# Kernel tuning notes

Measured on AMD Instinct MI355X. Metric: run time of the kernel, lower is better.

The kernel has to match this reference:

```python
import jax, jax.numpy as jnp
import numpy as np

EPS = 1e-6
GROUPS = 32


def group_norm(x, scale, bias):
    # x: [b, c, d, h, w]
    b, c, d, h, w = x.shape
    xg = x.reshape(b, GROUPS, c // GROUPS, d, h, w)
    mean = xg.mean(axis=(2, 3, 4, 5), keepdims=True)
    var = xg.var(axis=(2, 3, 4, 5), keepdims=True)
    xn = ((xg - mean) * jax.lax.rsqrt(var + EPS)).reshape(b, c, d, h, w)
    return xn * scale[None, :, None, None, None] + bias[None, :, None, None, None]


def setup_inputs() -> dict:
    key = jax.random.key(0)
    ks = jax.random.split(key, 6)
    C = 512
    x = jax.random.normal(ks[0], (2, C, 16, 16, 16), dtype=jnp.float32)
    s = 1.0 / np.sqrt(C)
    return {
        "x": x,
        "gn_scale": jnp.ones((C,), jnp.float32),
        "gn_bias": jnp.zeros((C,), jnp.float32),
        "wq": jax.random.normal(ks[1], (C, C), jnp.float32) * s,
        "bq": jnp.zeros((C,), jnp.float32),
        "wk": jax.random.normal(ks[2], (C, C), jnp.float32) * s,
        "bk": jnp.zeros((C,), jnp.float32),
        "wv": jax.random.normal(ks[3], (C, C), jnp.float32) * s,
        "bv": jnp.zeros((C,), jnp.float32),
        "wproj": jax.random.normal(ks[4], (C, C), jnp.float32) * s,
        "bproj": jnp.zeros((C,), jnp.float32),
    }


def reference(x, gn_scale, gn_bias, wq, bq, wk, bk, wv, bv, wproj, bproj):
    b, c, d, h, w = x.shape
    h_ = group_norm(x, gn_scale, gn_bias)
    hf = h_.reshape(b, c, d * h * w)  # [b, c, N]
    # 1x1x1 convs == per-position channel matmuls
    q = jnp.einsum("oc,bcn->bon", wq, hf) + bq[None, :, None]
    k = jnp.einsum("oc,bcn->bon", wk, hf) + bk[None, :, None]
    v = jnp.einsum("oc,bcn->bon", wv, hf) + bv[None, :, None]
    # attn[b, i, j] = softmax_j(q_i . k_j / sqrt(c))
    attn = jnp.einsum("bci,bcj->bij", q, k) * (c ** -0.5)
    attn = jax.nn.softmax(attn, axis=-1)
    # out[b, c, i] = sum_j v[b, c, j] * attn[b, i, j]
    out = jnp.einsum("bcj,bij->bci", v, attn)
    out = jnp.einsum("oc,bcn->bon", wproj, out) + bproj[None, :, None]
    return x + out.reshape(b, c, d, h, w)
```

## Files before the change

kernel.cpp:

```cpp
#include <hip/hip_runtime.h>
#include <hip/hip_bf16.h>

#define BB 2
#define CC 512
#define GG 32
#define NN 4096
#define EPSV 1e-6f

typedef __attribute__((ext_vector_type(4))) float f32x4;
typedef __attribute__((ext_vector_type(8))) short s16x8;
typedef __attribute__((ext_vector_type(4))) short s16x4;

__device__ __forceinline__ ushort f2bf(float f){
  union { float f; unsigned u; } v; v.f = f;
  unsigned r = v.u + 0x7fffu + ((v.u >> 16) & 1u);
  return (ushort)(r >> 16);
}
__device__ __forceinline__ short f2bfs(float f){ return (short)f2bf(f); }
__device__ __forceinline__ float b2f(ushort u){
  union { unsigned u; float f; } v; v.u = ((unsigned)u) << 16; return v.f;
}

__device__ __forceinline__ f32x4 mfma16(s16x8 a, s16x8 b, f32x4 c){
  return __builtin_amdgcn_mfma_f32_16x16x32_bf16(a, b, c, 0, 0, 0);
}

#define GLOAD_LDS16(g, l) __builtin_amdgcn_global_load_lds( \
    (const __attribute__((address_space(1))) void*)(g),     \
    (__attribute__((address_space(3))) void*)(l), 16, 0, 0)

__global__ __launch_bounds__(256) void k_prep(const float* __restrict__ wq, const float* __restrict__ wk,
                                              const float* __restrict__ wv, const float* __restrict__ wp,
                                              ushort* __restrict__ wbf,
                                              const float* __restrict__ x, float* __restrict__ pstat){
  if (blockIdx.x >= 256){
    int idx = (blockIdx.x - 256) * 256 + threadIdx.x;
    const float* srcs[4] = {wq, wk, wv, wp};
    #pragma unroll
    for (int m = 0; m < 4; m++){
      float4 v = reinterpret_cast<const float4*>(srcs[m])[idx];
      ushort4 o; o.x = f2bf(v.x); o.y = f2bf(v.y); o.z = f2bf(v.z); o.w = f2bf(v.w);
      reinterpret_cast<ushort4*>(wbf + (size_t)m * CC * CC)[idx] = o;
    }
    return;
  }
  int blk = blockIdx.x;
  const float* p = x + (size_t)blk * 16384;
  float s = 0.f, ss = 0.f;
  for (int i = threadIdx.x; i < 4096; i += 256){
    float4 v = reinterpret_cast<const float4*>(p)[i];
    s  += v.x + v.y + v.z + v.w;
    ss += v.x*v.x + v.y*v.y + v.z*v.z + v.w*v.w;
  }
  #pragma unroll
  for (int off = 32; off; off >>= 1){ s += __shfl_down(s, off); ss += __shfl_down(ss, off); }
  __shared__ float rs_[4], rss_[4];
  int w = threadIdx.x >> 6, lane = threadIdx.x & 63;
  if (lane == 0){ rs_[w] = s; rss_[w] = ss; }
  __syncthreads();
  if (threadIdx.x == 0){
    pstat[blk * 2 + 0] = rs_[0] + rs_[1] + rs_[2] + rs_[3];
    pstat[blk * 2 + 1] = rss_[0] + rss_[1] + rss_[2] + rss_[3];
  }
}

__global__ __launch_bounds__(256) void k_gn_apply(const float* __restrict__ x, const float* __restrict__ gsc,
                                                  const float* __restrict__ gbi, const float* __restrict__ pstat,
                                                  ushort* __restrict__ hf){
  __shared__ ushort tr[32][520];
  __shared__ float stl[64];
  int b = blockIdx.y;
  int nb = blockIdx.x * 32;
  int t = threadIdx.x;
  if (t < 32){
    float s = 0.f, ss = 0.f;
    #pragma unroll
    for (int k = 0; k < 4; k++){
      s  += pstat[(b * 128 + t * 4 + k) * 2 + 0];
      ss += pstat[(b * 128 + t * 4 + k) * 2 + 1];
    }
    float inv = 1.0f / (16.0f * NN);
    float mean = s * inv;
    float var = ss * inv - mean * mean;
    stl[t * 2 + 0] = mean;
    stl[t * 2 + 1] = rsqrtf(var + EPSV);
  }
  __syncthreads();
  int n = t & 31, cr = t >> 5;
  const float* xb = x + (size_t)b * CC * NN;
  for (int c0 = 0; c0 < CC; c0 += 8){
    int c = c0 + cr;
    float mean = stl[(c >> 4) * 2 + 0];
    float rstd = stl[(c >> 4) * 2 + 1];
    float v = xb[(size_t)c * NN + nb + n];
    tr[n][c] = f2bf((v - mean) * rstd * gsc[c] + gbi[c]);
  }
  __syncthreads();
  ushort* out = hf + ((size_t)b * NN + nb) * CC;
  int c8 = (t & 63) * 8;
  int nrow0 = t >> 6;
  #pragma unroll
  for (int i = 0; i < 8; i++){
    int nr = nrow0 + i * 4;
    *reinterpret_cast<s16x8*>(&out[(size_t)nr * CC + c8]) =
      *reinterpret_cast<const s16x8*>(&tr[nr][c8]);
  }
}

__global__ __launch_bounds__(256, 3) void k_gemm_qkv2(const ushort* __restrict__ W, const ushort* __restrict__ Bt,
                                                      const float* __restrict__ bq, const float* __restrict__ bk,
                                                      const float* __restrict__ bv,
                                                      ushort* __restrict__ qo, ushort* __restrict__ ko,
                                                      ushort* __restrict__ vo, float rs){
  __shared__ __align__(16) char smem[40960];
  __shared__ float bl[3][64];
  int b = blockIdx.z, ob = blockIdx.y * 64, nb = blockIdx.x * 128;
  int t = threadIdx.x, w = t >> 6, l = t & 63;
  int lr = l & 15, lk = l >> 4;
  int wo = (w >> 1) * 32, wn = (w & 1) * 64;
  if (t < 64){ bl[0][t] = bq[ob + t]; bl[1][t] = bk[ob + t]; bl[2][t] = bv[ob + t]; }
  const ushort* Bp = Bt + ((size_t)b * NN + nb) * CC;
  const ushort* Wp = W + (size_t)ob * CC;
  int srow = l >> 2;
  int schunk = (l & 3) ^ ((l >> 2) & 3) ^ ((l >> 4) & 3);
  int xs = (lk ^ (lr & 3) ^ ((lr >> 2) & 3)) * 8;

#define STAGE_QKV(BUF, K0)                                                               \
  {                                                                                      \
    ushort* As_ = (ushort*)(smem + (BUF) * 20480);                                       \
    ushort* Bs_ = As_ + 6144;                                                            \
    _Pragma("unroll")                                                                    \
    for (int tt = 0; tt < 5; tt++){                                                      \
      int inst = w * 5 + tt;                                                             \
      if (inst < 12){                                                                    \
        int m = inst >> 2, sub = inst & 3;                                               \
        const ushort* src = Wp + (size_t)m * CC * CC + (size_t)(sub * 16 + srow) * CC + (K0) + schunk * 8; \
        GLOAD_LDS16(src, As_ + m * 2048 + sub * 512);                                    \
      } else {                                                                           \
        int q = inst - 12;                                                               \
        const ushort* src = Bp + (size_t)(q * 16 + srow) * CC + (K0) + schunk * 8;       \
        GLOAD_LDS16(src, Bs_ + q * 512);                                                 \
      }                                                                                  \
    }                                                                                    \
  }

  f32x4 acc[3][2][4] = {};
  STAGE_QKV(0, 0)
  __syncthreads();
  for (int s16 = 0; s16 < 16; s16++){
    if (s16 < 15) STAGE_QKV((s16 + 1) & 1, (s16 + 1) * 32)
    const ushort* As = (const ushort*)(smem + (s16 & 1) * 20480);
    const ushort* Bs = As + 6144;
    s16x8 bf[4];
    #pragma unroll
    for (int sn = 0; sn < 4; sn++)
      bf[sn] = *(const s16x8*)&Bs[(wn + sn * 16 + lr) * 32 + xs];
    #pragma unroll
    for (int m = 0; m < 3; m++){
      s16x8 a0 = *(const s16x8*)&As[m * 2048 + (wo + lr) * 32 + xs];
      s16x8 a1 = *(const s16x8*)&As[m * 2048 + (wo + 16 + lr) * 32 + xs];
      #pragma unroll
      for (int sn = 0; sn < 4; sn++){
        acc[m][0][sn] = mfma16(a0, bf[sn], acc[m][0][sn]);
        acc[m][1][sn] = mfma16(a1, bf[sn], acc[m][1][sn]);
      }
    }
    __syncthreads();
  }
#undef STAGE_QKV
  #pragma unroll
  for (int m = 0; m < 2; m++){
    ushort* dst = (m == 0) ? qo : ko;
    float scl = (m == 0) ? rs : 1.0f;
    #pragma unroll
    for (int so = 0; so < 2; so++)
      #pragma unroll
      for (int sn = 0; sn < 4; sn++){
        int o0 = wo + so * 16 + lk * 4;
        int n  = nb + wn + sn * 16 + lr;
        s16x4 pv;
        #pragma unroll
        for (int r = 0; r < 4; r++) pv[r] = f2bfs((acc[m][so][sn][r] + bl[m][o0 + r]) * scl);
        *reinterpret_cast<s16x4*>(&dst[((size_t)b * NN + n) * CC + ob + o0]) = pv;
      }
  }
  ushort* Ve = (ushort*)smem;
  #pragma unroll
  for (int so = 0; so < 2; so++)
    #pragma unroll
    for (int sn = 0; sn < 4; sn++){
      int o0 = wo + so * 16 + lk * 4;
      int ncl = wn + sn * 16 + lr;
      #pragma unroll
      for (int r = 0; r < 4; r++) Ve[(o0 + r) * 136 + ncl] = f2bf(acc[2][so][sn][r] + bl[2][o0 + r]);
    }
  __syncthreads();
  {
    int row = t >> 2, cs = (t & 3) * 32;
    ushort* dst = &vo[((size_t)b * CC + ob + row) * NN + nb + cs];
    #pragma unroll
    for (int k = 0; k < 4; k++)
      *(s16x8*)&dst[k * 8] = *(const s16x8*)&Ve[row * 136 + cs + k * 8];
  }
}

__global__ __launch_bounds__(512, 2) void k_gemm_s(const ushort* __restrict__ qt, const ushort* __restrict__ kt,
                                                   ushort* __restrict__ P, float* __restrict__ part){
  extern __shared__ __align__(16) char smem[];
  int lin = blockIdx.x + 16 * blockIdx.y + 256 * blockIdx.z;
  int tt0 = (lin & 7) * 64 + (lin >> 3);
  int jblk = tt0 & 15;
  int pair = tt0 >> 4;
  int b = pair >> 4;
  int j0 = jblk * 256, i0 = (pair & 15) * 256;
  int t = threadIdx.x, w = t >> 6, l = t & 63;
  int lr = l & 15, lk = l >> 4;
  int wj2 = w >> 2, wi4 = w & 3;
  const ushort* kb = kt + ((size_t)b * NN + j0) * CC;
  const ushort* qb = qt + ((size_t)b * NN + i0) * CC;
  int srow = l >> 3;
  int schunk = (l & 7) ^ srow;

#define STAGE_KH(BUF, K0, H)                                                      \
  {                                                                               \
    ushort* D = (ushort*)(smem + (BUF) * 32768);                                  \
    _Pragma("unroll")                                                             \
    for (int tt = 0; tt < 2; tt++){                                               \
      int g = (H) * 16 + w * 2 + tt;                                              \
      const ushort* src = kb + (size_t)(g * 8 + srow) * CC + (K0) + schunk * 8;   \
      GLOAD_LDS16(src, D + g * 512);                                              \
    }                                                                             \
  }
#define STAGE_QH(BUF, K0, H)                                                      \
  {                                                                               \
    ushort* D = (ushort*)(smem + 65536 + (BUF) * 32768);                          \
    _Pragma("unroll")                                                             \
    for (int tt = 0; tt < 2; tt++){                                               \
      int g = (H) * 16 + w * 2 + tt;                                              \
      const ushort* src = qb + (size_t)(g * 8 + srow) * CC + (K0) + schunk * 8;   \
      GLOAD_LDS16(src, D + g * 512);                                              \
    }                                                                             \
  }
#define PHASE(SJ, STAGE_CODE)                                                     \
  {                                                                               \
    s16x8 a00 = *(const s16x8*)&Ks[(wj2 * 128 + (SJ) * 16 + lr) * 64 + xs0];      \
    s16x8 a01 = *(const s16x8*)&Ks[(wj2 * 128 + (SJ) * 16 + lr) * 64 + xs1];      \
    s16x8 a10 = *(const s16x8*)&Ks[(wj2 * 128 + ((SJ) + 1) * 16 + lr) * 64 + xs0];\
    s16x8 a11 = *(const s16x8*)&Ks[(wj2 * 128 + ((SJ) + 1) * 16 + lr) * 64 + xs1];\
    STAGE_CODE                                                                    \
    __builtin_amdgcn_s_barrier();                                                 \
    asm volatile("s_waitcnt lgkmcnt(0)" ::: "memory");                            \
    __builtin_amdgcn_sched_barrier(0);                                            \
    __builtin_amdgcn_s_setprio(1);                                                \
    _Pragma("unroll")                                                             \
    for (int si = 0; si < 4; si++){                                               \
      acc[SJ][si]       = mfma16(a00, bq[si][0], acc[SJ][si]);                    \
      acc[SJ][si]       = mfma16(a01, bq[si][1], acc[SJ][si]);                    \
      acc[(SJ) + 1][si] = mfma16(a10, bq[si][0], acc[(SJ) + 1][si]);              \
      acc[(SJ) + 1][si] = mfma16(a11, bq[si][1], acc[(SJ) + 1][si]);              \
    }                                                                             \
    __builtin_amdgcn_s_setprio(0);                                                \
    __builtin_amdgcn_s_barrier();                                                 \
  }

  f32x4 acc[8][4] = {};
  STAGE_KH(0, 0, 0)
  STAGE_KH(0, 0, 1)
  STAGE_QH(0, 0, 0)
  STAGE_QH(0, 0, 1)
  STAGE_QH(1, 64, 0)
  STAGE_QH(1, 64, 1)
  #pragma unroll
  for (int s8 = 0; s8 < 8; s8++){
    const int tau = s8 & 1;
    const ushort* Ks = (const ushort*)(smem + tau * 32768);
    const ushort* Qs = (const ushort*)(smem + 65536 + tau * 32768);
    if (s8 < 7){ asm volatile("s_waitcnt vmcnt(4)" ::: "memory"); }
    else       { asm volatile("s_waitcnt vmcnt(0)" ::: "memory"); }
    __builtin_amdgcn_s_barrier();
    __builtin_amdgcn_sched_barrier(0);
    int xs0 = (lk ^ (lr & 7)) * 8;
    int xs1 = ((4 + lk) ^ (lr & 7)) * 8;
    s16x8 bq[4][2];
    #pragma unroll
    for (int si = 0; si < 4; si++){
      bq[si][0] = *(const s16x8*)&Qs[(wi4 * 64 + si * 16 + lr) * 64 + xs0];
      bq[si][1] = *(const s16x8*)&Qs[(wi4 * 64 + si * 16 + lr) * 64 + xs1];
    }
    PHASE(0, if (s8 < 7) STAGE_KH(tau ^ 1, (s8 + 1) * 64, 0))
    PHASE(2, if (s8 < 7) STAGE_KH(tau ^ 1, (s8 + 1) * 64, 1))
    PHASE(4, if (s8 < 6) STAGE_QH(tau, (s8 + 2) * 64, 0))
    PHASE(6, if (s8 < 6) STAGE_QH(tau, (s8 + 2) * 64, 1))
  }
#undef PHASE
#undef STAGE_KH
#undef STAGE_QH
  ushort* Pe = (ushort*)smem;
  float rsum[4] = {0.f, 0.f, 0.f, 0.f};
  #pragma unroll
  for (int pass = 0; pass < 2; pass++){
    if ((wi4 >> 1) == pass){
      #pragma unroll
      for (int sj = 0; sj < 8; sj++)
        #pragma unroll
        for (int si = 0; si < 4; si++){
          int il = (wi4 & 1) * 64 + si * 16 + lr;
          int jl = wj2 * 128 + sj * 16 + lk * 4;
          s16x4 pk;
          #pragma unroll
          for (int r = 0; r < 4; r++){
            float e = __builtin_amdgcn_exp2f(acc[sj][si][r]);
            pk[r] = f2bfs(e);
            rsum[si] += e;
          }
          *(s16x4*)&Pe[il * 264 + jl] = pk;
        }
    }
    __syncthreads();
    {
      int row = t >> 2, cs = (t & 3) * 64;
      ushort* dst = P + ((size_t)b * NN + i0 + pass * 128 + row) * NN + j0 + cs;
      #pragma unroll
      for (int k = 0; k < 8; k++)
        *(s16x8*)&dst[k * 8] = *(const s16x8*)&Pe[row * 264 + cs + k * 8];
    }
    __syncthreads();
  }
  #pragma unroll
  for (int si = 0; si < 4; si++){
    float s = rsum[si];
    s += __shfl_xor(s, 16);
    s += __shfl_xor(s, 32);
    if (lk == 0){
      int il = wi4 * 64 + si * 16 + lr;
      part[((size_t)b * NN + i0 + il) * 32 + jblk * 2 + wj2] = s;
    }
  }
}

__global__ __launch_bounds__(512) void k_gemm_o(const ushort* __restrict__ P, const ushort* __restrict__ vv,
                                                const float* __restrict__ part, ushort* __restrict__ ot){
  __shared__ __align__(16) char smem[65536];
  int lin = blockIdx.x + 4 * blockIdx.y + 128 * blockIdx.z;
  int tt0 = (lin & 7) * 32 + (lin >> 3);
  int cblk = tt0 & 3;
  int ib   = tt0 >> 2;
  int b = ib >> 5;
  int c0 = cblk * 128, i0 = (ib & 31) * 128;
  int t = threadIdx.x, w = t >> 6, l = t & 63;
  int lr = l & 15, lk = l >> 4;
  int wi2 = w >> 2, wc4 = w & 3;
  const ushort* vb = vv + ((size_t)b * CC + c0) * NN;
  const ushort* pb = P + ((size_t)b * NN + i0) * NN;
  int srow = l >> 3;
  int schunk = (l & 7) ^ srow;

#define STAGE_V(BUF, K0)                                                          \
  {                                                                               \
    ushort* D = (ushort*)(smem + (BUF) * 16384);                                  \
    _Pragma("unroll")                                                             \
    for (int tt = 0; tt < 2; tt++){                                               \
      int g = w * 2 + tt;                                                         \
      const ushort* src = vb + (size_t)(g * 8 + srow) * NN + (K0) + schunk * 8;   \
      GLOAD_LDS16(src, D + g * 512);                                              \
    }                                                                             \
  }
#define STAGE_P(BUF, K0)                                                          \
  {                                                                               \
    ushort* D = (ushort*)(smem + 32768 + (BUF) * 16384);                          \
    _Pragma("unroll")                                                             \
    for (int tt = 0; tt < 2; tt++){                                               \
      int g = w * 2 + tt;                                                         \
      const ushort* src = pb + (size_t)(g * 8 + srow) * NN + (K0) + schunk * 8;   \
      GLOAD_LDS16(src, D + g * 512);                                              \
    }                                                                             \
  }

  f32x4 acc[2][4] = {};
  STAGE_V(0, 0)
  STAGE_P(0, 0)
  STAGE_P(1, 64)
  for (int s64 = 0; s64 < 64; s64++){
    const int tau = s64 & 1;
    const ushort* Vs = (const ushort*)(smem + tau * 16384);
    const ushort* Ps = (const ushort*)(smem + 32768 + tau * 16384);
    if (s64 < 63){ asm volatile("s_waitcnt vmcnt(2)" ::: "memory"); }
    else         { asm volatile("s_waitcnt vmcnt(0)" ::: "memory"); }
    __builtin_amdgcn_s_barrier();
    __builtin_amdgcn_sched_barrier(0);
    int xs0 = (lk ^ (lr & 7)) * 8;
    int xs1 = ((4 + lk) ^ (lr & 7)) * 8;
    s16x8 bf[4][2];
    #pragma unroll
    for (int si = 0; si < 4; si++){
      bf[si][0] = *(const s16x8*)&Ps[(wi2 * 64 + si * 16 + lr) * 64 + xs0];
      bf[si][1] = *(const s16x8*)&Ps[(wi2 * 64 + si * 16 + lr) * 64 + xs1];
    }
    {
      s16x8 af0 = *(const s16x8*)&Vs[(wc4 * 32 + lr) * 64 + xs0];
      s16x8 af1 = *(const s16x8*)&Vs[(wc4 * 32 + 16 + lr) * 64 + xs0];
      if (s64 < 63) STAGE_V(tau ^ 1, (s64 + 1) * 64)
      __builtin_amdgcn_s_barrier();
      asm volatile("s_waitcnt lgkmcnt(0)" ::: "memory");
      __builtin_amdgcn_sched_barrier(0);
      __builtin_amdgcn_s_setprio(1);
      #pragma unroll
      for (int si = 0; si < 4; si++){
        acc[0][si] = mfma16(af0, bf[si][0], acc[0][si]);
        acc[1][si] = mfma16(af1, bf[si][0], acc[1][si]);
      }
      __builtin_amdgcn_s_setprio(0);
      __builtin_amdgcn_s_barrier();
    }
    {
      s16x8 af0 = *(const s16x8*)&Vs[(wc4 * 32 + lr) * 64 + xs1];
      s16x8 af1 = *(const s16x8*)&Vs[(wc4 * 32 + 16 + lr) * 64 + xs1];
      if (s64 < 62) STAGE_P(tau, (s64 + 2) * 64)
      __builtin_amdgcn_s_barrier();
      asm volatile("s_waitcnt lgkmcnt(0)" ::: "memory");
      __builtin_amdgcn_sched_barrier(0);
      __builtin_amdgcn_s_setprio(1);
      #pragma unroll
      for (int si = 0; si < 4; si++){
        acc[0][si] = mfma16(af0, bf[si][1], acc[0][si]);
        acc[1][si] = mfma16(af1, bf[si][1], acc[1][si]);
      }
      __builtin_amdgcn_s_setprio(0);
      __builtin_amdgcn_s_barrier();
    }
  }
#undef STAGE_V
#undef STAGE_P
  ushort* Oe = (ushort*)smem;
  float* linv_lds = (float*)(smem + 34816);
  if (t < 128){
    const float* pp = part + ((size_t)b * NN + i0 + t) * 32;
    float s = 0.f;
    #pragma unroll
    for (int k = 0; k < 32; k++) s += pp[k];
    linv_lds[t] = 1.0f / s;
  }
  __syncthreads();
  #pragma unroll
  for (int si = 0; si < 4; si++){
    int il = wi2 * 64 + si * 16 + lr;
    float li = linv_lds[il];
    #pragma unroll
    for (int sc = 0; sc < 2; sc++){
      int cl = wc4 * 32 + sc * 16 + lk * 4;
      s16x4 pk;
      #pragma unroll
      for (int r = 0; r < 4; r++) pk[r] = f2bfs(acc[sc][si][r] * li);
      *(s16x4*)&Oe[il * 136 + cl] = pk;
    }
  }
  __syncthreads();
  {
    int row = t >> 2, cs = (t & 3) * 32;
    ushort* dst = ot + ((size_t)b * NN + i0 + row) * CC + c0 + cs;
    #pragma unroll
    for (int k = 0; k < 4; k++)
      *(s16x8*)&dst[k * 8] = *(const s16x8*)&Oe[row * 136 + cs + k * 8];
  }
}

__global__ __launch_bounds__(256, 3) void k_gemm_proj2(const ushort* __restrict__ A, const ushort* __restrict__ Bt,
                                                       const float* __restrict__ bias, float* __restrict__ o32,
                                                       const float* __restrict__ xres){
  __shared__ __align__(16) char smem[34048];
  __shared__ float bl[64];
  int b = blockIdx.z, ob = blockIdx.y * 64, nb = blockIdx.x * 128;
  int t = threadIdx.x, w = t >> 6, l = t & 63;
  int lr = l & 15, lk = l >> 4;
  int wo = (w >> 1) * 32, wn = (w & 1) * 64;
  if (t < 64) bl[t] = bias[ob + t];
  const ushort* Bp = Bt + ((size_t)b * NN + nb) * CC;
  const ushort* Ap = A + (size_t)ob * CC;
  int srow = l >> 2;
  int schunk = (l & 3) ^ ((l >> 2) & 3) ^ ((l >> 4) & 3);
  int xs = (lk ^ (lr & 3) ^ ((lr >> 2) & 3)) * 8;

#define STAGE_P2(BUF, K0)                                                         \
  {                                                                               \
    ushort* As_ = (ushort*)(smem + (BUF) * 12288);                                \
    ushort* Bs_ = As_ + 2048;                                                     \
    _Pragma("unroll")                                                             \
    for (int tt = 0; tt < 3; tt++){                                               \
      int inst = w * 3 + tt;                                                      \
      if (inst < 4){                                                              \
        const ushort* src = Ap + (size_t)(inst * 16 + srow) * CC + (K0) + schunk * 8; \
        GLOAD_LDS16(src, As_ + inst * 512);                                       \
      } else {                                                                    \
        int q = inst - 4;                                                         \
        const ushort* src = Bp + (size_t)(q * 16 + srow) * CC + (K0) + schunk * 8; \
        GLOAD_LDS16(src, Bs_ + q * 512);                                          \
      }                                                                           \
    }                                                                             \
  }

  f32x4 acc[2][4] = {};
  STAGE_P2(0, 0)
  __syncthreads();
  for (int s16 = 0; s16 < 16; s16++){
    if (s16 < 15) STAGE_P2((s16 + 1) & 1, (s16 + 1) * 32)
    const ushort* As = (const ushort*)(smem + (s16 & 1) * 12288);
    const ushort* Bs = As + 2048;
    s16x8 a0 = *(const s16x8*)&As[(wo + lr) * 32 + xs];
    s16x8 a1 = *(const s16x8*)&As[(wo + 16 + lr) * 32 + xs];
    #pragma unroll
    for (int sn = 0; sn < 4; sn++){
      s16x8 bf = *(const s16x8*)&Bs[(wn + sn * 16 + lr) * 32 + xs];
      acc[0][sn] = mfma16(a0, bf, acc[0][sn]);
      acc[1][sn] = mfma16(a1, bf, acc[1][sn]);
    }
    __syncthreads();
  }
#undef STAGE_P2
  float* trf = (float*)smem;
  #pragma unroll
  for (int so = 0; so < 2; so++)
    #pragma unroll
    for (int sn = 0; sn < 4; sn++){
      int o0 = wo + so * 16 + lk * 4;
      int ncl = wn + sn * 16 + lr;
      #pragma unroll
      for (int r = 0; r < 4; r++) trf[(o0 + r) * 133 + ncl] = acc[so][sn][r] + bl[o0 + r];
    }
  __syncthreads();
  {
    int row = t >> 2, cs = (t & 3) * 32;
    size_t base = ((size_t)b * CC + ob + row) * NN + nb + cs;
    #pragma unroll
    for (int q = 0; q < 8; q++){
      float4 xv = *reinterpret_cast<const float4*>(&xres[base + q * 4]);
      float4 ov;
      ov.x = xv.x + trf[row * 133 + cs + q * 4 + 0];
      ov.y = xv.y + trf[row * 133 + cs + q * 4 + 1];
      ov.z = xv.z + trf[row * 133 + cs + q * 4 + 2];
      ov.w = xv.w + trf[row * 133 + cs + q * 4 + 3];
      *reinterpret_cast<float4*>(&o32[base + q * 4]) = ov;
    }
  }
}

extern "C" void kernel_launch(void* const* d_in, const int* in_sizes, int n_in,
                              void* d_out, int out_size, void* d_ws, size_t ws_size,
                              hipStream_t stream){
  const float* x   = (const float*)d_in[0];
  const float* gsc = (const float*)d_in[1];
  const float* gbi = (const float*)d_in[2];
  const float* wq  = (const float*)d_in[3];
  const float* bq  = (const float*)d_in[4];
  const float* wk  = (const float*)d_in[5];
  const float* bk  = (const float*)d_in[6];
  const float* wv  = (const float*)d_in[7];
  const float* bv  = (const float*)d_in[8];
  const float* wp  = (const float*)d_in[9];
  const float* bp  = (const float*)d_in[10];
  char* ws = (char*)d_ws;
  const size_t MB = 1024 * 1024;
  ushort* wbf  = (ushort*)ws;
  ushort* qtb  = (ushort*)(ws + 2 * MB);
  ushort* ktb  = (ushort*)(ws + 10 * MB);
  ushort* vvb  = (ushort*)(ws + 18 * MB);
  ushort* hfb  = (ushort*)(ws + 26 * MB);
  ushort* Pbuf = (ushort*)(ws + 34 * MB);
  float* pstat = (float*)(ws + 98 * MB);
  float* part  = (float*)(ws + 26 * MB);
  ushort* otb  = qtb;

  const float rs = 0.044194173824159216f * 1.4426950408889634f;

  k_prep<<<512, 256, 0, stream>>>(wq, wk, wv, wp, wbf, x, pstat);
  k_gn_apply<<<dim3(128, 2, 1), 256, 0, stream>>>(x, gsc, gbi, pstat, hfb);
  k_gemm_qkv2<<<dim3(32, 8, 2), 256, 0, stream>>>(wbf, hfb, bq, bk, bv, qtb, ktb, vvb, rs);
  k_gemm_s<<<dim3(16, 16, 2), 512, 131072, stream>>>(qtb, ktb, Pbuf, part);
  k_gemm_o<<<dim3(4, 32, 2), 512, 0, stream>>>(Pbuf, vvb, part, otb);
  k_gemm_proj2<<<dim3(32, 8, 2), 256, 0, stream>>>(wbf + 3 * CC * CC, otb, bp, (float*)d_out, x);
}
```

Before: 166.2 us.

## Triple-buffer P tiles in PV GEMM and collapse per-step barriers to one

The P operand in k_gemm_o moves from double to triple buffering in shared memory, with a rotating buffer index. This lets each 64-wide k step load all V and P fragments up front, issue the next V and P prefetches, and run all MFMAs in one block. The step now needs only the single barrier at its top instead of several intra-step barriers. The cost is 16KB more LDS per block (80KB total), which could limit occupancy, plus a trailing __syncthreads before the shared memory is reused for the epilogue.

```diff
diff --git a/kernel.cpp b/kernel.cpp
--- a/kernel.cpp
+++ b/kernel.cpp
@@ -340,7 +340,7 @@
 
 __global__ __launch_bounds__(512) void k_gemm_o(const ushort* __restrict__ P, const ushort* __restrict__ vv,
                                                 const float* __restrict__ part, ushort* __restrict__ ot){
-  __shared__ __align__(16) char smem[65536];
+  __shared__ __align__(16) char smem[81920];
   int lin = blockIdx.x + 4 * blockIdx.y + 128 * blockIdx.z;
   int tt0 = (lin & 7) * 32 + (lin >> 3);
   int cblk = tt0 & 3;
@@ -380,57 +380,47 @@
   STAGE_V(0, 0)
   STAGE_P(0, 0)
   STAGE_P(1, 64)
+  int pcur = 0;
   for (int s64 = 0; s64 < 64; s64++){
-    const int tau = s64 & 1;
-    const ushort* Vs = (const ushort*)(smem + tau * 16384);
-    const ushort* Ps = (const ushort*)(smem + 32768 + tau * 16384);
+    const ushort* Vs = (const ushort*)(smem + (s64 & 1) * 16384);
+    const ushort* Ps = (const ushort*)(smem + 32768 + pcur * 16384);
     if (s64 < 63){ asm volatile("s_waitcnt vmcnt(2)" ::: "memory"); }
     else         { asm volatile("s_waitcnt vmcnt(0)" ::: "memory"); }
     __builtin_amdgcn_s_barrier();
     __builtin_amdgcn_sched_barrier(0);
     int xs0 = (lk ^ (lr & 7)) * 8;
     int xs1 = ((4 + lk) ^ (lr & 7)) * 8;
-    s16x8 bf[4][2];
+    s16x8 bf[4][2], af0k0, af1k0, af0k1, af1k1;
     #pragma unroll
     for (int si = 0; si < 4; si++){
       bf[si][0] = *(const s16x8*)&Ps[(wi2 * 64 + si * 16 + lr) * 64 + xs0];
       bf[si][1] = *(const s16x8*)&Ps[(wi2 * 64 + si * 16 + lr) * 64 + xs1];
     }
+    af0k0 = *(const s16x8*)&Vs[(wc4 * 32 + lr) * 64 + xs0];
+    af1k0 = *(const s16x8*)&Vs[(wc4 * 32 + 16 + lr) * 64 + xs0];
+    af0k1 = *(const s16x8*)&Vs[(wc4 * 32 + lr) * 64 + xs1];
+    af1k1 = *(const s16x8*)&Vs[(wc4 * 32 + 16 + lr) * 64 + xs1];
+    if (s64 < 63) STAGE_V((s64 + 1) & 1, (s64 + 1) * 64)
     {
-      s16x8 af0 = *(const s16x8*)&Vs[(wc4 * 32 + lr) * 64 + xs0];
-      s16x8 af1 = *(const s16x8*)&Vs[(wc4 * 32 + 16 + lr) * 64 + xs0];
-      if (s64 < 63) STAGE_V(tau ^ 1, (s64 + 1) * 64)
-      __builtin_amdgcn_s_barrier();
-      asm volatile("s_waitcnt lgkmcnt(0)" ::: "memory");
-      __builtin_amdgcn_sched_barrier(0);
-      __builtin_amdgcn_s_setprio(1);
-      #pragma unroll
-      for (int si = 0; si < 4; si++){
-        acc[0][si] = mfma16(af0, bf[si][0], acc[0][si]);
-        acc[1][si] = mfma16(af1, bf[si][0], acc[1][si]);
-      }
-      __builtin_amdgcn_s_setprio(0);
-      __builtin_amdgcn_s_barrier();
-    }
-    {
-      s16x8 af0 = *(const s16x8*)&Vs[(wc4 * 32 + lr) * 64 + xs1];
-      s16x8 af1 = *(const s16x8*)&Vs[(wc4 * 32 + 16 + lr) * 64 + xs1];
-      if (s64 < 62) STAGE_P(tau, (s64 + 2) * 64)
-      __builtin_amdgcn_s_barrier();
-      asm volatile("s_waitcnt lgkmcnt(0)" ::: "memory");
-      __builtin_amdgcn_sched_barrier(0);
-      __builtin_amdgcn_s_setprio(1);
-      #pragma unroll
-      for (int si = 0; si < 4; si++){
-        acc[0][si] = mfma16(af0, bf[si][1], acc[0][si]);
-        acc[1][si] = mfma16(af1, bf[si][1], acc[1][si]);
-      }
-      __builtin_amdgcn_s_setprio(0);
-      __builtin_amdgcn_s_barrier();
-    }
+      int pnxt = pcur + 2; if (pnxt >= 3) pnxt -= 3;
+      if (s64 < 62) STAGE_P(pnxt, (s64 + 2) * 64)
+    }
+    asm volatile("s_waitcnt lgkmcnt(0)" ::: "memory");
+    __builtin_amdgcn_sched_barrier(0);
+    __builtin_amdgcn_s_setprio(1);
+    #pragma unroll
+    for (int si = 0; si < 4; si++){
+      acc[0][si] = mfma16(af0k0, bf[si][0], acc[0][si]);
+      acc[1][si] = mfma16(af1k0, bf[si][0], acc[1][si]);
+      acc[0][si] = mfma16(af0k1, bf[si][1], acc[0][si]);
+      acc[1][si] = mfma16(af1k1, bf[si][1], acc[1][si]);
+    }
+    __builtin_amdgcn_s_setprio(0);
+    pcur = pcur + 1; if (pcur >= 3) pcur = 0;
   }
 #undef STAGE_V
 #undef STAGE_P
+  __syncthreads();
   ushort* Oe = (ushort*)smem;
   float* linv_lds = (float*)(smem + 34816);
   if (t < 128){
```

New measurement: 171.1 us. 1.03x slower.
